# Performance work log

Measured on AMD Instinct MI355X. Metric: run time of the kernel, lower is better.

Reference implementation:

```python
import math
import jax, jax.numpy as jnp
import numpy as np

B, T, QDIM, ADIM = 256, 2048, 1024, 128
DC, DK = 8, 21          # dynamic channels / kernel
SC, SK = 8, 21          # static channels / kernel
PL, ALPHA, BETA = 11, 0.1, 0.9


def _betabinom_pmf_flipped(n, a, b, length):
    lg = np.vectorize(math.lgamma)
    k = np.arange(length, dtype=np.float64)
    logp = (lg(n + 1.0) - lg(k + 1.0) - lg(n - k + 1.0)
            + lg(k + a) + lg(n - k + b) - lg(n + a + b)
            - (lg(a) + lg(b) - lg(a + b)))
    return np.exp(logp)[::-1].copy()  # .flip(0) as in the torch buffer


def setup_inputs() -> dict:
    key = jax.random.key(0)
    ks = jax.random.split(key, 10)

    def lin(k, shape, fan_in):
        return (jax.random.normal(k, shape, jnp.float32) / np.sqrt(fan_in)).astype(jnp.float32)

    query = jax.random.normal(ks[0], (B, QDIM), jnp.float32)
    # previous-step alignment: a valid probability distribution over T
    alignment_pre = jax.nn.softmax(2.0 * jax.random.normal(ks[1], (B, T), jnp.float32), axis=1)

    P = jnp.asarray(_betabinom_pmf_flipped(PL - 1, ALPHA, BETA, PL), jnp.float32)
    W_w = lin(ks[2], (ADIM, QDIM), QDIM)
    W_b = jnp.zeros((ADIM,), jnp.float32)
    V_w = lin(ks[3], (DC * DK, ADIM), ADIM)
    F_w = lin(ks[4], (SC, 1, SK), SK)        # Conv1d(1, SC, SK) weight
    U_w = lin(ks[5], (ADIM, SC), SC)
    T_w = lin(ks[6], (ADIM, DC), DC)
    T_b = jnp.zeros((ADIM,), jnp.float32)
    v_w = lin(ks[7], (1, ADIM), ADIM)
    return {"query": query, "alignment_pre": alignment_pre, "P": P,
            "W_w": W_w, "W_b": W_b, "V_w": V_w, "F_w": F_w,
            "U_w": U_w, "T_w": T_w, "T_b": T_b, "v_w": v_w}


def reference(query, alignment_pre, P, W_w, W_b, V_w, F_w, U_w, T_w, T_b, v_w):
    b, t = alignment_pre.shape
    pad = (DK - 1) // 2  # == PL - 1 == 10, shared by all three convs
    x_pad = jnp.pad(alignment_pre, ((0, 0), (pad, pad)))
    # sliding windows (cross-correlation layout): windows[b, t, k] = x_pad[b, t + k]
    windows = jnp.stack([x_pad[:, k:k + t] for k in range(DK)], axis=-1)  # (B, T, DK)

    # prior: causal conv with left pad PL-1 == windows taps 0..PL-1
    p = jnp.log(jnp.clip(jnp.einsum('btk,k->bt', windows[..., :PL], P), 1e-6))

    # per-sample dynamic kernels
    G = jnp.tanh(query @ W_w.T + W_b) @ V_w.T          # (B, DC*DK)
    G = G.reshape(b, DC, DK)
    g = jnp.einsum('btk,bck->btc', windows, G)          # grouped conv, groups=B -> (B, T, DC)

    # static conv over previous alignment
    f = jnp.einsum('btk,ck->btc', windows, F_w[:, 0, :])  # (B, T, SC)

    e = jnp.squeeze(jnp.tanh(f @ U_w.T + g @ T_w.T + T_b) @ v_w.T, -1) + p  # (B, T)
    return jax.nn.softmax(e, axis=1)
```

## Files before the change

kernel.cpp:

```cpp
#include <hip/hip_runtime.h>
#include <hip/hip_bf16.h>

#define Bsz 256
#define Tn 2048
#define QD 1024
#define AD 128
#define DCn 8
#define DKn 21
#define PLn 11
#define GN (DCn * DKn)

typedef _Float16 f16x8 __attribute__((ext_vector_type(8)));
typedef float f32x4 __attribute__((ext_vector_type(4)));
typedef unsigned int u32;

#define TWO_LOG2E 2.8853900817779268f

__device__ __forceinline__ u32 pkh_rne(float a, float b) {
    union { _Float16 h[2]; u32 u; } p;
    p.h[0] = (_Float16)a; p.h[1] = (_Float16)b;
    return p.u;
}

__global__ __launch_bounds__(1024, 4) void dca_kernel(
    const float* __restrict__ query, const float* __restrict__ align,
    const float* __restrict__ P, const float* __restrict__ W_w,
    const float* __restrict__ W_b, const float* __restrict__ V_w,
    const float* __restrict__ F_w, const float* __restrict__ U_w,
    const float* __restrict__ T_w, const float* __restrict__ T_b,
    const float* __restrict__ v_w, float* __restrict__ out)
{
    __shared__ __align__(16) _Float16 al16[Tn + 44];
    __shared__ float    pcb[Tn];
    __shared__ float    sden[Tn];
    __shared__ __align__(16) float h_lds[AD];
    __shared__ float    G_lds[GN];
    __shared__ float    red[16];
    __shared__ float    bc;

    const int b    = blockIdx.x;
    const int tid  = threadIdx.x;
    const int lane = tid & 63;
    const int wid  = tid >> 6;
    const int l15  = lane & 15;
    const int quad = lane >> 4;

    if (tid < 512) {
        float4 v = ((const float4*)(align + (size_t)b * Tn))[tid];
        u32* dst = (u32*)&al16[10 + tid * 4];
        dst[0] = pkh_rne(v.x, v.y);
        dst[1] = pkh_rne(v.z, v.w);
    } else if (tid < 576) {
        int k = tid - 512;
        if (k < 10)       al16[k]      = (_Float16)0.f;
        else if (k < 44)  al16[Tn + k] = (_Float16)0.f;
    }

    {
        const float4* q4 = (const float4*)(query + (size_t)b * QD);
        float4 q0 = q4[lane];
        float4 q1 = q4[64 + lane];
        float4 q2 = q4[128 + lane];
        float4 q3 = q4[192 + lane];
        #pragma unroll 2
        for (int i = 0; i < 8; ++i) {
            int a = wid * 8 + i;
            const float4* w4 = (const float4*)(W_w + (size_t)a * QD);
            float4 x0 = w4[lane];
            float4 x1 = w4[64 + lane];
            float4 x2 = w4[128 + lane];
            float4 x3 = w4[192 + lane];
            float accA = 0.f, accB = 0.f;
            accA = fmaf(q0.x, x0.x, fmaf(q0.y, x0.y, fmaf(q0.z, x0.z, fmaf(q0.w, x0.w, accA))));
            accB = fmaf(q1.x, x1.x, fmaf(q1.y, x1.y, fmaf(q1.z, x1.z, fmaf(q1.w, x1.w, accB))));
            accA = fmaf(q2.x, x2.x, fmaf(q2.y, x2.y, fmaf(q2.z, x2.z, fmaf(q2.w, x2.w, accA))));
            accB = fmaf(q3.x, x3.x, fmaf(q3.y, x3.y, fmaf(q3.z, x3.z, fmaf(q3.w, x3.w, accB))));
            float acc = accA + accB;
            #pragma unroll
            for (int off = 32; off; off >>= 1) acc += __shfl_xor(acc, off);
            if (lane == 0) h_lds[a] = tanhf(acc + W_b[a]);
        }
    }
    __syncthreads();

    if (tid < 4 * GN) {
        const int r = tid >> 2;
        const int s = tid & 3;
        const float4* v4 = (const float4*)(V_w + (size_t)r * AD + s * 32);
        const float4* h4 = (const float4*)(h_lds + s * 32);
        float g = 0.f;
        #pragma unroll
        for (int i = 0; i < 8; ++i) {
            float4 vv = v4[i];
            float4 hh = h4[i];
            g = fmaf(vv.x, hh.x, fmaf(vv.y, hh.y, fmaf(vv.z, hh.z, fmaf(vv.w, hh.w, g))));
        }
        g += __shfl_xor(g, 1);
        g += __shfl_xor(g, 2);
        if (s == 0) G_lds[r] = g;
    }

    const int t0w = wid * 128;
    #pragma unroll
    for (int tt = 0; tt < 2; ++tt) {
        int t = t0w + tt * 64 + lane;
        float pr = 0.f;
        #pragma unroll
        for (int k = 0; k < PLn; ++k) pr = fmaf((float)al16[t + k], P[k], pr);
        pcb[t] = fmaxf(pr, 1e-6f);
    }

    f16x8 Bf[8];
    #pragma unroll
    for (int n = 0; n < 8; ++n) {
        int a = n * 16 + l15;
        f16x8 bf = {};
        if (quad < 2) {
            const float* src = (quad == 0) ? (U_w + a * 8) : (T_w + a * 8);
            float4 lo = ((const float4*)src)[0];
            float4 hi = ((const float4*)src)[1];
            bf[0] = (_Float16)(TWO_LOG2E * lo.x); bf[1] = (_Float16)(TWO_LOG2E * lo.y);
            bf[2] = (_Float16)(TWO_LOG2E * lo.z); bf[3] = (_Float16)(TWO_LOG2E * lo.w);
            bf[4] = (_Float16)(TWO_LOG2E * hi.x); bf[5] = (_Float16)(TWO_LOG2E * hi.y);
            bf[6] = (_Float16)(TWO_LOG2E * hi.z); bf[7] = (_Float16)(TWO_LOG2E * hi.w);
        } else if (quad == 2) {
            bf[0] = (_Float16)(TWO_LOG2E * T_b[a]);
        }
        Bf[n] = bf;
    }

    f32x4 vnq[8];
    float vsum = 0.f;
    #pragma unroll
    for (int n = 0; n < 8; ++n) {
        f32x4 vq = *(const f32x4*)(v_w + n * 16 + quad * 4);
        vsum += vq[0] + vq[1] + vq[2] + vq[3];
        vq[0] *= -2.f; vq[1] *= -2.f; vq[2] *= -2.f; vq[3] *= -2.f;
        vnq[n] = vq;
    }
    vsum += __shfl_xor(vsum, 16);
    vsum += __shfl_xor(vsum, 32);

    f16x8 Ac0, Ac1;
    #pragma unroll
    for (int j = 0; j < 8; ++j) {
        Ac0[j] = al16[t0w      + l15 + quad * 8 + j];
        Ac1[j] = al16[t0w + 16 + l15 + quad * 8 + j];
    }

    __syncthreads();

    f16x8 Bc = {};
    #pragma unroll
    for (int j = 0; j < 8; ++j) {
        int k = quad * 8 + j;
        float wv = 0.f;
        if (k < DKn) wv = (l15 < 8) ? F_w[l15 * DKn + k]
                                    : G_lds[(l15 - 8) * DKn + k];
        Bc[j] = (_Float16)wv;
    }

    const int addrA = ((((lane & 48) << 1) | (lane & 15)) << 2);
    const int addrB = addrA + 64;

    float wsum = 0.f;

    #pragma unroll 1
    for (int m = 0; m < 8; m += 2) {
        const int ta  = t0w + m * 16;
        const int tb_ = ta + 16;

        f32x4 z = {};
        f32x4 X0 = __builtin_amdgcn_mfma_f32_16x16x32_f16(Bc, Ac0, z, 0, 0, 0);
        f32x4 X1 = __builtin_amdgcn_mfma_f32_16x16x32_f16(Bc, Ac1, z, 0, 0, 0);

        if (m < 6) {
            #pragma unroll
            for (int j = 0; j < 8; ++j) {
                Ac0[j] = al16[ta  + 32 + l15 + quad * 8 + j];
                Ac1[j] = al16[tb_ + 32 + l15 + quad * 8 + j];
            }
        }

        u32 lo0 = pkh_rne(X0[0], X0[1]), hi0 = pkh_rne(X0[2], X0[3]);
        u32 lo1 = pkh_rne(X1[0], X1[1]), hi1 = pkh_rne(X1[2], X1[3]);

        union { u32 w[4]; f16x8 v; } U0, U1;
        U0.w[0] = (u32)__builtin_amdgcn_ds_bpermute(addrA, (int)lo0);
        U0.w[1] = (u32)__builtin_amdgcn_ds_bpermute(addrA, (int)hi0);
        U0.w[2] = (u32)__builtin_amdgcn_ds_bpermute(addrB, (int)lo0);
        U0.w[3] = (u32)__builtin_amdgcn_ds_bpermute(addrB, (int)hi0);
        U1.w[0] = (u32)__builtin_amdgcn_ds_bpermute(addrA, (int)lo1);
        U1.w[1] = (u32)__builtin_amdgcn_ds_bpermute(addrA, (int)hi1);
        U1.w[2] = (u32)__builtin_amdgcn_ds_bpermute(addrB, (int)lo1);
        U1.w[3] = (u32)__builtin_amdgcn_ds_bpermute(addrB, (int)hi1);
        if (quad == 2) {
            U0.w[0] = 0x3C00u;
            U1.w[0] = 0x3C00u;
        }

        float es0 = 0.f, es1 = 0.f;
        #pragma unroll
        for (int n = 0; n < 8; ++n) {
            f32x4 z2 = {};
            f32x4 d0 = __builtin_amdgcn_mfma_f32_16x16x32_f16(Bf[n], U0.v, z2, 0, 0, 0);
            f32x4 d1 = __builtin_amdgcn_mfma_f32_16x16x32_f16(Bf[n], U1.v, z2, 0, 0, 0);
            #pragma unroll
            for (int r = 0; r < 4; ++r) {
                float qa = __builtin_amdgcn_exp2f(d0[r]);
                float qb = __builtin_amdgcn_exp2f(d1[r]);
                float ra = __builtin_amdgcn_rcpf(qa + 1.f);
                float rb = __builtin_amdgcn_rcpf(qb + 1.f);
                es0 = fmaf(vnq[n][r], ra, es0);
                es1 = fmaf(vnq[n][r], rb, es1);
            }
        }
        es0 += __shfl_xor(es0, 16);
        es0 += __shfl_xor(es0, 32);
        es1 += __shfl_xor(es1, 16);
        es1 += __shfl_xor(es1, 32);

        if (lane < 32) {
            int t    = ((lane < 16) ? ta : tb_) + l15;
            float e  = (lane < 16) ? es0 : es1;
            float sv = pcb[t] * __expf(e + vsum);
            sden[t] = sv;
            wsum += sv;
        }
    }

    __syncthreads();
    #pragma unroll
    for (int off = 32; off; off >>= 1) wsum += __shfl_xor(wsum, off);
    if (lane == 0) red[wid] = wsum;
    __syncthreads();
    if (wid == 0) {
        float ss = (lane < 16) ? red[lane] : 0.f;
        #pragma unroll
        for (int off = 8; off; off >>= 1) ss += __shfl_xor(ss, off);
        if (lane == 0) bc = ss;
    }
    __syncthreads();
    const float inv = 1.f / bc;
    out[b * Tn + tid]        = sden[tid] * inv;
    out[b * Tn + tid + 1024] = sden[tid + 1024] * inv;
}

extern "C" void kernel_launch(void* const* d_in, const int* in_sizes, int n_in,
                              void* d_out, int out_size, void* d_ws, size_t ws_size,
                              hipStream_t stream) {
    const float* query = (const float*)d_in[0];
    const float* align = (const float*)d_in[1];
    const float* P     = (const float*)d_in[2];
    const float* W_w   = (const float*)d_in[3];
    const float* W_b   = (const float*)d_in[4];
    const float* V_w   = (const float*)d_in[5];
    const float* F_w   = (const float*)d_in[6];
    const float* U_w   = (const float*)d_in[7];
    const float* T_w   = (const float*)d_in[8];
    const float* T_b   = (const float*)d_in[9];
    const float* v_w   = (const float*)d_in[10];
    float* out = (float*)d_out;

    dca_kernel<<<Bsz, 1024, 0, stream>>>(query, align, P, W_w, W_b, V_w,
                                         F_w, U_w, T_w, T_b, v_w, out);
}
```

Before: 105.7 us.

## Fold static and dynamic conv weights into one per-sample 128x21 kernel matrix

The kernel no longer runs two chained matmuls per time tile (window×conv weights, then ×U/T). It first builds, per block with one MFMA per wave, a combined matrix M = U·F + T·G with the bias folded into an extra column, and stores it in LDS. The main loop then multiplies the raw alignment windows by M directly. This removes the first MFMA pair, the fp16 repacking and the eight ds_bpermute shuffles from every iteration. The cost is an extra 8 KB of LDS, an added barrier, non-prefetched window loads inside the loop, and a different fp16 rounding point for the fused weights.

```diff
diff --git a/kernel.cpp b/kernel.cpp
--- a/kernel.cpp
+++ b/kernel.cpp
@@ -9,6 +9,7 @@
 #define DKn 21
 #define PLn 11
 #define GN (DCn * DKn)
+#define MS 32
 
 typedef _Float16 f16x8 __attribute__((ext_vector_type(8)));
 typedef float f32x4 __attribute__((ext_vector_type(4)));
@@ -35,6 +36,7 @@
     __shared__ float    sden[Tn];
     __shared__ __align__(16) float h_lds[AD];
     __shared__ float    G_lds[GN];
+    __shared__ __align__(16) _Float16 M16[AD * MS];
     __shared__ float    red[16];
     __shared__ float    bc;
 
@@ -110,25 +112,6 @@
         pcb[t] = fmaxf(pr, 1e-6f);
     }
 
-    f16x8 Bf[8];
-    #pragma unroll
-    for (int n = 0; n < 8; ++n) {
-        int a = n * 16 + l15;
-        f16x8 bf = {};
-        if (quad < 2) {
-            const float* src = (quad == 0) ? (U_w + a * 8) : (T_w + a * 8);
-            float4 lo = ((const float4*)src)[0];
-            float4 hi = ((const float4*)src)[1];
-            bf[0] = (_Float16)(TWO_LOG2E * lo.x); bf[1] = (_Float16)(TWO_LOG2E * lo.y);
-            bf[2] = (_Float16)(TWO_LOG2E * lo.z); bf[3] = (_Float16)(TWO_LOG2E * lo.w);
-            bf[4] = (_Float16)(TWO_LOG2E * hi.x); bf[5] = (_Float16)(TWO_LOG2E * hi.y);
-            bf[6] = (_Float16)(TWO_LOG2E * hi.z); bf[7] = (_Float16)(TWO_LOG2E * hi.w);
-        } else if (quad == 2) {
-            bf[0] = (_Float16)(TWO_LOG2E * T_b[a]);
-        }
-        Bf[n] = bf;
-    }
-
     f32x4 vnq[8];
     float vsum = 0.f;
     #pragma unroll
@@ -141,27 +124,50 @@
     vsum += __shfl_xor(vsum, 16);
     vsum += __shfl_xor(vsum, 32);
 
-    f16x8 Ac0, Ac1;
-    #pragma unroll
-    for (int j = 0; j < 8; ++j) {
-        Ac0[j] = al16[t0w      + l15 + quad * 8 + j];
-        Ac1[j] = al16[t0w + 16 + l15 + quad * 8 + j];
-    }
-
-    __syncthreads();
-
-    f16x8 Bc = {};
-    #pragma unroll
-    for (int j = 0; j < 8; ++j) {
-        int k = quad * 8 + j;
-        float wv = 0.f;
-        if (k < DKn) wv = (l15 < 8) ? F_w[l15 * DKn + k]
-                                    : G_lds[(l15 - 8) * DKn + k];
-        Bc[j] = (_Float16)wv;
-    }
-
-    const int addrA = ((((lane & 48) << 1) | (lane & 15)) << 2);
-    const int addrB = addrA + 64;
+    const int atile = wid & 7;
+    const int ktile = wid >> 3;
+    const int kcol  = ktile * 16 + l15;
+
+    f16x8 Am = {};
+    if (quad < 2) {
+        const int a = atile * 16 + l15;
+        const float* src = (quad == 0) ? (U_w + a * 8) : (T_w + a * 8);
+        float4 lo = ((const float4*)src)[0];
+        float4 hi = ((const float4*)src)[1];
+        Am[0] = (_Float16)lo.x; Am[1] = (_Float16)lo.y;
+        Am[2] = (_Float16)lo.z; Am[3] = (_Float16)lo.w;
+        Am[4] = (_Float16)hi.x; Am[5] = (_Float16)hi.y;
+        Am[6] = (_Float16)hi.z; Am[7] = (_Float16)hi.w;
+    }
+    f16x8 Bm = {};
+    if (quad == 0 && kcol < DKn) {
+        #pragma unroll
+        for (int j = 0; j < 8; ++j) Bm[j] = (_Float16)F_w[j * DKn + kcol];
+    }
+
+    __syncthreads();
+
+    if (quad == 1 && kcol < DKn) {
+        #pragma unroll
+        for (int j = 0; j < 8; ++j) Bm[j] = (_Float16)G_lds[j * DKn + kcol];
+    }
+    {
+        f32x4 z = {};
+        f32x4 Dm = __builtin_amdgcn_mfma_f32_16x16x32_f16(Am, Bm, z, 0, 0, 0);
+        #pragma unroll
+        for (int r = 0; r < 4; ++r) {
+            int a = atile * 16 + quad * 4 + r;
+            float val = TWO_LOG2E * Dm[r];
+            if (ktile == 1 && l15 == 5) val = TWO_LOG2E * T_b[a];
+            M16[a * MS + kcol] = (_Float16)val;
+        }
+    }
+    __syncthreads();
+
+    f16x8 Mf[8];
+    #pragma unroll
+    for (int n = 0; n < 8; ++n)
+        Mf[n] = *(const f16x8*)&M16[(n * 16 + l15) * MS + quad * 8];
 
     float wsum = 0.f;
 
@@ -170,41 +176,23 @@
         const int ta  = t0w + m * 16;
         const int tb_ = ta + 16;
 
-        f32x4 z = {};
-        f32x4 X0 = __builtin_amdgcn_mfma_f32_16x16x32_f16(Bc, Ac0, z, 0, 0, 0);
-        f32x4 X1 = __builtin_amdgcn_mfma_f32_16x16x32_f16(Bc, Ac1, z, 0, 0, 0);
-
-        if (m < 6) {
-            #pragma unroll
-            for (int j = 0; j < 8; ++j) {
-                Ac0[j] = al16[ta  + 32 + l15 + quad * 8 + j];
-                Ac1[j] = al16[tb_ + 32 + l15 + quad * 8 + j];
-            }
-        }
-
-        u32 lo0 = pkh_rne(X0[0], X0[1]), hi0 = pkh_rne(X0[2], X0[3]);
-        u32 lo1 = pkh_rne(X1[0], X1[1]), hi1 = pkh_rne(X1[2], X1[3]);
-
-        union { u32 w[4]; f16x8 v; } U0, U1;
-        U0.w[0] = (u32)__builtin_amdgcn_ds_bpermute(addrA, (int)lo0);
-        U0.w[1] = (u32)__builtin_amdgcn_ds_bpermute(addrA, (int)hi0);
-        U0.w[2] = (u32)__builtin_amdgcn_ds_bpermute(addrB, (int)lo0);
-        U0.w[3] = (u32)__builtin_amdgcn_ds_bpermute(addrB, (int)hi0);
-        U1.w[0] = (u32)__builtin_amdgcn_ds_bpermute(addrA, (int)lo1);
-        U1.w[1] = (u32)__builtin_amdgcn_ds_bpermute(addrA, (int)hi1);
-        U1.w[2] = (u32)__builtin_amdgcn_ds_bpermute(addrB, (int)lo1);
-        U1.w[3] = (u32)__builtin_amdgcn_ds_bpermute(addrB, (int)hi1);
+        f16x8 Ac0, Ac1;
+        #pragma unroll
+        for (int j = 0; j < 8; ++j) {
+            Ac0[j] = al16[ta  + l15 + quad * 8 + j];
+            Ac1[j] = al16[tb_ + l15 + quad * 8 + j];
+        }
         if (quad == 2) {
-            U0.w[0] = 0x3C00u;
-            U1.w[0] = 0x3C00u;
+            Ac0[5] = (_Float16)1.f;
+            Ac1[5] = (_Float16)1.f;
         }
 
         float es0 = 0.f, es1 = 0.f;
         #pragma unroll
         for (int n = 0; n < 8; ++n) {
             f32x4 z2 = {};
-            f32x4 d0 = __builtin_amdgcn_mfma_f32_16x16x32_f16(Bf[n], U0.v, z2, 0, 0, 0);
-            f32x4 d1 = __builtin_amdgcn_mfma_f32_16x16x32_f16(Bf[n], U1.v, z2, 0, 0, 0);
+            f32x4 d0 = __builtin_amdgcn_mfma_f32_16x16x32_f16(Mf[n], Ac0, z2, 0, 0, 0);
+            f32x4 d1 = __builtin_amdgcn_mfma_f32_16x16x32_f16(Mf[n], Ac1, z2, 0, 0, 0);
             #pragma unroll
             for (int r = 0; r < 4; ++r) {
                 float qa = __builtin_amdgcn_exp2f(d0[r]);
```

After: 100.6 us. 4.8% less time.
